# Optimization experiments

Hardware: AMD Instinct MI355X
Metric: run time of the kernel (lower is better)

Reference implementation:

```python
import jax, jax.numpy as jnp
import numpy as np

D_SINGLE = 384
D_PAIR = 128
D_HID = 16
H = 12
PQ = 4
PV = 8
EPS = 1e-8


def setup_inputs() -> dict:
    key = jax.random.key(0)
    ks = jax.random.split(key, 12)
    B, N = 1, 768
    w = lambda k, shp: jax.random.normal(k, shp, dtype=jnp.float32) * 0.02
    hc = H * D_HID
    concat_dim = H * (D_PAIR + D_HID + PV * 4)
    return {
        's': jax.random.normal(ks[0], (B, N, D_SINGLE), dtype=jnp.float32),
        'z': jax.random.normal(ks[1], (B, N, N, D_PAIR), dtype=jnp.float32),
        'square_mask': jnp.zeros((B, 1, N, N), dtype=jnp.float32),
        'rot': jax.random.normal(ks[2], (B, N, 3, 3), dtype=jnp.float32),
        'trans': jax.random.normal(ks[3], (B, N, 3), dtype=jnp.float32),
        'Wq': w(ks[4], (D_SINGLE, hc)), 'bq': jnp.zeros((hc,), jnp.float32),
        'Wkv': w(ks[5], (D_SINGLE, 2 * hc)), 'bkv': jnp.zeros((2 * hc,), jnp.float32),
        'Wqp': w(ks[6], (D_SINGLE, H * PQ * 3)), 'bqp': jnp.zeros((H * PQ * 3,), jnp.float32),
        'Wkvp': w(ks[7], (D_SINGLE, H * (PQ + PV) * 3)), 'bkvp': jnp.zeros((H * (PQ + PV) * 3,), jnp.float32),
        'Wb': w(ks[8], (D_PAIR, H)), 'bb': jnp.zeros((H,), jnp.float32),
        'head_weights': jnp.zeros((H,), jnp.float32),
        'Wout': w(ks[9], (concat_dim, D_SINGLE)), 'bout': jnp.zeros((D_SINGLE,), jnp.float32),
    }


def _ipa(s, z, square_mask, rot, trans, Wq, bq, Wkv, bkv, Wqp, bqp, Wkvp, bkvp,
         Wb, bb, head_weights, Wout, bout):
    B, N, _ = s.shape
    # scalar q/k/v
    q = (s @ Wq + bq).reshape(B, N, H, D_HID)
    kv = (s @ Wkv + bkv).reshape(B, N, H, 2 * D_HID)
    k, v = kv[..., :D_HID], kv[..., D_HID:]

    def frame_apply(pts):  # pts [B,N,K,3] -> R @ p + t per residue
        return jnp.einsum('bnij,bnkj->bnki', rot, pts) + trans[:, :, None, :]

    def to_points(raw):  # [B,N,3K] coordinate-major -> [B,N,K,3]
        x, y, zc = jnp.split(raw, 3, axis=-1)
        return jnp.stack([x, y, zc], axis=-1)

    q_pts = frame_apply(to_points(s @ Wqp + bqp)).reshape(B, N, H, PQ, 3)
    kv_pts = frame_apply(to_points(s @ Wkvp + bkvp)).reshape(B, N, H, PQ + PV, 3)
    k_pts, v_pts = kv_pts[..., :PQ, :], kv_pts[..., PQ:, :]

    # scalar attention + pair bias
    bias = z @ Wb + bb  # [B,N,N,H]
    attn = jnp.einsum('bqhd,bkhd->bhqk', q, k) * np.sqrt(1.0 / (3 * D_HID))
    attn = attn + np.sqrt(1.0 / 3) * jnp.transpose(bias, (0, 3, 1, 2))

    # point-distance attention
    diff = q_pts[:, :, None] - k_pts[:, None]          # [B,Nq,Nk,H,PQ,3]
    d2 = jnp.sum(diff * diff, axis=-1)                  # [B,Nq,Nk,H,PQ]
    hw = jax.nn.softplus(head_weights) * np.sqrt(1.0 / (3 * (PQ * 9.0 / 2)))
    pt_att = -0.5 * jnp.sum(d2 * hw[None, None, None, :, None], axis=-1)  # [B,Nq,Nk,H]

    attn = attn + square_mask + jnp.transpose(pt_att, (0, 3, 1, 2))
    attn = jax.nn.softmax(attn, axis=-1)                # [B,H,Nq,Nk]

    # aggregation
    o = jnp.einsum('bhqk,bkhd->bqhd', attn, v).reshape(B, N, H * D_HID)
    o_pts = jnp.einsum('bhqk,bkhpc->bqhpc', attn, v_pts)           # [B,N,H,PV,3]
    o_pair = jnp.einsum('bhqk,bqkc->bqhc', attn, z).reshape(B, N, H * D_PAIR)

    # invert frames: R^T (p - t)
    o_pts = jnp.einsum('bnji,bnhpj->bnhpi', rot, o_pts - trans[:, :, None, None, :])
    o_pts_norm = jnp.sqrt(jnp.sum(o_pts * o_pts, axis=-1) + EPS).reshape(B, N, H * PV)
    o_pts_flat = o_pts.reshape(B, N, H * PV, 3)

    cat = jnp.concatenate(
        [o, o_pts_flat[..., 0], o_pts_flat[..., 1], o_pts_flat[..., 2], o_pts_norm, o_pair],
        axis=-1)
    return cat @ Wout + bout


def reference(s, z, square_mask, rot, trans, Wq, bq, Wkv, bkv, Wqp, bqp, Wkvp,
              bkvp, Wb, bb, head_weights, Wout, bout):
    return _ipa(s, z, square_mask, rot, trans, Wq, bq, Wkv, bkv, Wqp, bqp,
                Wkvp, bkvp, Wb, bb, head_weights, Wout, bout)
```

## Files before the change

kernel.cpp:

```cpp
#include <hip/hip_runtime.h>
#include <hip/hip_bf16.h>
#include <math.h>

#define N_RES 768
#define DS 384
#define DP 128
#define DH 16
#define NH 12
#define PQ 4
#define PV 8
#define HC (NH*DH)
#define CATD (NH*(DP+DH+PV*4))
#define BK 64
#define NSPLIT 2
#define KRANGE (N_RES/NSPLIT)
#define PSTRIDE 2048
#define ZST 140

typedef __attribute__((ext_vector_type(8))) short bf16x8;
typedef __attribute__((ext_vector_type(4))) float f32x4;

#define WS_Q     0
#define WS_KT    (WS_Q + N_RES*HC)
#define WS_QP    (WS_KT + NH*N_RES*DH)
#define WS_KPT   (WS_QP + N_RES*144)
#define WS_KPSQ  (WS_KPT + NH*N_RES*12)
#define WS_RAWQ  (WS_KPSQ + NH*N_RES)
#define WS_RAWKV (WS_RAWQ + N_RES*144)
#define WS_VT    (WS_RAWKV + N_RES*432)
#define WS_VPT   (WS_VT + 192*N_RES/2)
#define WS_CATB  (WS_VPT + 288*N_RES/2)
#define WS_WOT   (WS_CATB + N_RES*CATD/2)
#define WS_PART  (WS_WOT + 384*CATD/2)
#define WS_SB    (WS_PART + N_RES*NSPLIT*PSTRIDE)
#define WS_WT    (WS_SB + 768*384/2)
#define WS_QA    (WS_WT + 1152*384/2)
#define WS_KB    (WS_QA + NH*N_RES*32/2)
#define WS_SP    (WS_KB + NH*N_RES*32/2)

__device__ __forceinline__ unsigned short f2b(float f) {
    union { __hip_bfloat16 b; unsigned short u; } c;
    c.b = __float2bfloat16(f);
    return c.u;
}
__device__ __forceinline__ float b2f(unsigned short u) {
    return __uint_as_float((unsigned)u << 16);
}

__global__ __launch_bounds__(384) void k_cvtall(
    const float* __restrict__ s,
    const float* __restrict__ Wq, const float* __restrict__ Wkv,
    const float* __restrict__ Wqp, const float* __restrict__ Wkvp,
    const float* __restrict__ Wout, float* __restrict__ ws)
{
    const int b = blockIdx.x, t = threadIdx.x;
    unsigned short* sb  = (unsigned short*)(ws + WS_SB);
    unsigned short* wt  = (unsigned short*)(ws + WS_WT);
    unsigned short* wot = (unsigned short*)(ws + WS_WOT);
    if (b < 768) {
        sb[(size_t)b * 384 + t] = f2b(s[(size_t)b * 384 + t]);
    } else if (b < 1920) {
        int j = b - 768;
        const float* W; int col, nc;
        if (j < 192)      { W = Wq;   col = j;       nc = 192; }
        else if (j < 576) { W = Wkv;  col = j - 192; nc = 384; }
        else if (j < 720) { W = Wqp;  col = j - 576; nc = 144; }
        else              { W = Wkvp; col = j - 720; nc = 432; }
        wt[(size_t)j * 384 + t] = f2b(W[(size_t)t * nc + col]);
    } else {
        int k = b - 1920;
        wot[(size_t)t * CATD + k] = f2b(Wout[(size_t)k * DS + t]);
    }
}

__global__ __launch_bounds__(256) void k_projm(
    const float* __restrict__ bq, const float* __restrict__ bkv,
    const float* __restrict__ bqp, const float* __restrict__ bkvp,
    float* __restrict__ ws)
{
    __shared__ float red[16][96];
    const int t = threadIdx.x;
    const int lane = t & 63;
    const int w = t >> 6;
    const int l15 = lane & 15;
    const int g = lane >> 4;
    const int m0 = blockIdx.x * 16;
    const int j0 = blockIdx.y * 96;
    const unsigned short* sb = (const unsigned short*)(ws + WS_SB);
    const unsigned short* wt = (const unsigned short*)(ws + WS_WT);
    unsigned short* vt = (unsigned short*)(ws + WS_VT);

    f32x4 acc[6];
    #pragma unroll
    for (int i = 0; i < 6; i++) acc[i] = (f32x4){0.f, 0.f, 0.f, 0.f};

    for (int ks = w; ks < 12; ks += 4) {
        int k0 = ks * 32;
        bf16x8 a = *(const bf16x8*)&sb[(size_t)(m0 + l15) * 384 + k0 + g * 8];
        #pragma unroll
        for (int ns = 0; ns < 6; ns++) {
            bf16x8 bfr = *(const bf16x8*)&wt[(size_t)(j0 + ns * 16 + l15) * 384 + k0 + g * 8];
            acc[ns] = __builtin_amdgcn_mfma_f32_16x16x32_bf16(a, bfr, acc[ns], 0, 0, 0);
        }
    }
    for (int idx = t; idx < 16 * 96; idx += 256) ((float*)red)[idx] = 0.f;
    __syncthreads();
    #pragma unroll
    for (int ns = 0; ns < 6; ns++)
        #pragma unroll
        for (int r = 0; r < 4; r++)
            atomicAdd(&red[g * 4 + r][ns * 16 + l15], acc[ns][r]);
    __syncthreads();

    for (int idx = t; idx < 16 * 96; idx += 256) {
        int row = idx / 96, c = idx % 96;
        int n = m0 + row, j = j0 + c;
        float v = red[row][c];
        if (j < 192) {
            ws[WS_Q + (size_t)n * HC + j] = v + bq[j];
        } else if (j < 576) {
            int jj = j - 192, h = jj / 32, dd = jj % 32;
            float vb = v + bkv[jj];
            if (dd < 16) ws[WS_KT + ((size_t)h * N_RES + n) * 16 + dd] = vb;
            else         vt[(size_t)(h * 16 + dd - 16) * N_RES + n] = f2b(vb);
        } else if (j < 720) {
            ws[WS_RAWQ + (size_t)n * 144 + (j - 576)] = v + bqp[j - 576];
        } else {
            ws[WS_RAWKV + (size_t)n * 432 + (j - 720)] = v + bkvp[j - 720];
        }
    }
}

__global__ __launch_bounds__(192) void k_frame(
    const float* __restrict__ rot, const float* __restrict__ trans,
    const float* __restrict__ hweights,
    float* __restrict__ ws)
{
    __shared__ float kpsq_s[NH];
    __shared__ float qp_f[144];
    __shared__ float kp_f[144];
    const int n = blockIdx.x;
    const int t = threadIdx.x;
    unsigned short* vpt = (unsigned short*)(ws + WS_VPT);
    unsigned short* qa  = (unsigned short*)(ws + WS_QA);
    unsigned short* kb  = (unsigned short*)(ws + WS_KB);
    if (t < NH) kpsq_s[t] = 0.f;
    __syncthreads();
    const float* R = rot + n * 9;
    const float* T = trans + n * 3;
    if (t < 48) {
        float x = ws[WS_RAWQ + (size_t)n * 144 + t];
        float y = ws[WS_RAWQ + (size_t)n * 144 + 48 + t];
        float z = ws[WS_RAWQ + (size_t)n * 144 + 96 + t];
        qp_f[t * 3 + 0] = R[0] * x + R[1] * y + R[2] * z + T[0];
        qp_f[t * 3 + 1] = R[3] * x + R[4] * y + R[5] * z + T[1];
        qp_f[t * 3 + 2] = R[6] * x + R[7] * y + R[8] * z + T[2];
    } else {
        int p2 = t - 48;
        float x = ws[WS_RAWKV + (size_t)n * 432 + p2];
        float y = ws[WS_RAWKV + (size_t)n * 432 + 144 + p2];
        float z = ws[WS_RAWKV + (size_t)n * 432 + 288 + p2];
        int h = p2 / 12, pp = p2 % 12;
        float fx = R[0] * x + R[1] * y + R[2] * z + T[0];
        float fy = R[3] * x + R[4] * y + R[5] * z + T[1];
        float fz = R[6] * x + R[7] * y + R[8] * z + T[2];
        if (pp < 4) {
            kp_f[h * 12 + pp * 3 + 0] = fx;
            kp_f[h * 12 + pp * 3 + 1] = fy;
            kp_f[h * 12 + pp * 3 + 2] = fz;
            atomicAdd(&kpsq_s[h], fx * fx + fy * fy + fz * fz);
        } else {
            size_t b = (size_t)(h * 24 + (pp - 4) * 3) * N_RES + n;
            vpt[b] = f2b(fx); vpt[b + N_RES] = f2b(fy); vpt[b + 2 * N_RES] = f2b(fz);
        }
    }
    __syncthreads();
    if (t < NH) ws[WS_KPSQ + (size_t)t * N_RES + n] = kpsq_s[t];
    for (int i = t; i < 768; i += 192) {
        int side = i / 384, idx = i % 384;
        int h = idx / 32, c = idx % 32;
        if (side == 0) {
            float hwv = log1pf(expf(hweights[h])) * 0.1360827635f;
            float v = (c < 16) ? ws[WS_Q + (size_t)n * HC + h * 16 + c] * 0.1443375673f
                    : ((c < 28) ? qp_f[h * 12 + (c - 16)] * hwv : 0.f);
            qa[((size_t)h * N_RES + n) * 32 + c] = f2b(v);
        } else {
            float v = (c < 16) ? ws[WS_KT + ((size_t)h * N_RES + n) * 16 + c]
                    : ((c < 28) ? kp_f[h * 12 + (c - 16)] : 0.f);
            kb[((size_t)h * N_RES + n) * 32 + c] = f2b(v);
        }
    }
}

__global__ __launch_bounds__(256) void k_logit(
    const float* __restrict__ mask, const float* __restrict__ bb,
    const float* __restrict__ hweights, float* __restrict__ ws)
{
    const int t = threadIdx.x;
    const int lane = t & 63;
    const int w = t >> 6;
    const int l15 = lane & 15;
    const int g = lane >> 4;
    const int q0 = blockIdx.x * 64 + w * 16;
    const int k0 = blockIdx.y * 96;
    const int h  = blockIdx.z;
    const unsigned short* qa = (const unsigned short*)(ws + WS_QA);
    const unsigned short* kb = (const unsigned short*)(ws + WS_KB);
    unsigned short* sp = (unsigned short*)(ws + WS_SP);

    float hwv = log1pf(expf(hweights[h])) * 0.1360827635f;
    float bbt = bb[h] * 0.5773502692f;

    bf16x8 a = *(const bf16x8*)&qa[((size_t)h * N_RES + q0 + l15) * 32 + g * 8];
    f32x4 acc[6];
    #pragma unroll
    for (int ns = 0; ns < 6; ns++) {
        bf16x8 bf = *(const bf16x8*)&kb[((size_t)h * N_RES + k0 + ns * 16 + l15) * 32 + g * 8];
        acc[ns] = __builtin_amdgcn_mfma_f32_16x16x32_bf16(
            a, bf, (f32x4){0.f, 0.f, 0.f, 0.f}, 0, 0, 0);
    }
    #pragma unroll
    for (int ns = 0; ns < 6; ns++) {
        int kk = k0 + ns * 16 + l15;
        float kq = ws[WS_KPSQ + (size_t)h * N_RES + kk];
        #pragma unroll
        for (int r = 0; r < 4; r++) {
            int qq = q0 + g * 4 + r;
            float v = acc[ns][r] + mask[(size_t)qq * N_RES + kk] + bbt - 0.5f * hwv * kq;
            sp[((size_t)h * N_RES + qq) * N_RES + kk] = f2b(v);
        }
    }
}

__global__ __launch_bounds__(256) void k_attn(
    const float* __restrict__ zg, const float* __restrict__ Wb,
    float* __restrict__ ws)
{
    __shared__ unsigned short z_s[2][BK][ZST];
    __shared__ unsigned short wb_lds[4][64][8];
    __shared__ unsigned short p_lds[16][72];
    __shared__ float b_lds[BK][13];
    __shared__ float r_s[16];

    const int t = threadIdx.x;
    const int lane = t & 63;
    const int w = t >> 6;
    const int l15 = lane & 15;
    const int g = lane >> 4;
    const int h0 = 3 * w;
    const int q  = blockIdx.x >> 1;
    const int ks = blockIdx.x & 1;
    const int kbase = ks * KRANGE;

    const float* zq = zg + ((size_t)q * N_RES + kbase) * DP;
    const unsigned short* VT  = (const unsigned short*)(ws + WS_VT);
    const unsigned short* VPT = (const unsigned short*)(ws + WS_VPT);
    const unsigned short* sp  = (const unsigned short*)(ws + WS_SP);

    for (int i = t; i < 16 * 72; i += 256) p_lds[i / 72][i % 72] = 0;
    if (t < 16) r_s[t] = 1.f;
    for (int i = t; i < 4 * 64 * 8; i += 256) {
        int j = i & 7, ln = (i >> 3) & 63, kc = i >> 9;
        int c = kc * 32 + ((ln >> 4) << 3) + j;
        int h = ln & 15;
        wb_lds[kc][ln][j] = (h < 12) ? f2b(Wb[c * NH + h] * 0.5773502692f)
                                     : (unsigned short)0;
    }
    {
        const float4* src = (const float4*)zq;
        #pragma unroll
        for (int i = 0; i < 8; i++) {
            int idx = i * 256 + t;
            float4 v = src[idx];
            unsigned u0 = (unsigned)f2b(v.x) | ((unsigned)f2b(v.y) << 16);
            unsigned u1 = (unsigned)f2b(v.z) | ((unsigned)f2b(v.w) << 16);
            *(unsigned long long*)&z_s[0][idx >> 5][(idx & 31) * 4] =
                (unsigned long long)u0 | ((unsigned long long)u1 << 32);
        }
    }

    float m_run[3], ssum[3];
    #pragma unroll
    for (int hl = 0; hl < 3; hl++) { m_run[hl] = -1e30f; ssum[hl] = 0.f; }

    f32x4 acc_op[2], acc_o[3], acc_pt[5];
    #pragma unroll
    for (int i = 0; i < 2; i++) acc_op[i] = (f32x4){0.f, 0.f, 0.f, 0.f};
    #pragma unroll
    for (int i = 0; i < 3; i++) acc_o[i] = (f32x4){0.f, 0.f, 0.f, 0.f};
    #pragma unroll
    for (int i = 0; i < 5; i++) acc_pt[i] = (f32x4){0.f, 0.f, 0.f, 0.f};

    __syncthreads();

    int cur = 0;
    for (int kb = 0; kb < KRANGE; kb += BK) {
        {
            f32x4 bacc = (f32x4){0.f, 0.f, 0.f, 0.f};
            #pragma unroll
            for (int kc = 0; kc < 4; kc++) {
                bf16x8 a = *(bf16x8*)&wb_lds[kc][lane][0];
                bf16x8 b = *(bf16x8*)&z_s[cur][w * 16 + l15][kc * 32 + g * 8];
                bacc = __builtin_amdgcn_mfma_f32_16x16x32_bf16(a, b, bacc, 0, 0, 0);
            }
            #pragma unroll
            for (int r = 0; r < 4; r++) {
                int h = g * 4 + r;
                if (h < 12) b_lds[w * 16 + l15][h] = bacc[r];
            }
        }
        __syncthreads();

        {
            const int kk = kbase + kb + lane;
            #pragma unroll
            for (int hl = 0; hl < 3; hl++) {
                int gh = h0 + hl;
                float dot = b_lds[lane][gh]
                          + b2f(sp[((size_t)gh * N_RES + q) * N_RES + kk]);
                float lm = dot;
                #pragma unroll
                for (int off = 32; off; off >>= 1) lm = fmaxf(lm, __shfl_xor(lm, off));
                float m_new = fmaxf(m_run[hl], lm);
                float rr = __expf(m_run[hl] - m_new);
                float p = __expf(dot - m_new);
                ssum[hl] = ssum[hl] * rr + p;
                m_run[hl] = m_new;
                p_lds[gh][lane] = f2b(p);
                if (lane == 0) r_s[gh] = rr;
            }
        }
        __syncthreads();

        const bool has_next = (kb + BK < KRANGE);
        const float4* src = (const float4*)(zq + (size_t)(kb + BK) * DP);
        float4 va[4];
        if (has_next) {
            #pragma unroll
            for (int i = 0; i < 4; i++) va[i] = src[i * 256 + t];
        }
        {
            bf16x8 pa0 = *(bf16x8*)&p_lds[l15][g * 8];
            bf16x8 pa1 = *(bf16x8*)&p_lds[l15][32 + g * 8];
            float rr0 = r_s[g * 4 + 0], rr1 = r_s[g * 4 + 1];
            float rr2 = r_s[g * 4 + 2], rr3 = r_s[g * 4 + 3];

            #pragma unroll
            for (int i = 0; i < 2; i++) {
                int c = (w * 2 + i) * 16 + l15;
                acc_op[i][0] *= rr0; acc_op[i][1] *= rr1;
                acc_op[i][2] *= rr2; acc_op[i][3] *= rr3;
                union { bf16x8 v; unsigned short u[8]; } b0, b1;
                #pragma unroll
                for (int j = 0; j < 8; j++) {
                    b0.u[j] = z_s[cur][g * 8 + j][c];
                    b1.u[j] = z_s[cur][32 + g * 8 + j][c];
                }
                acc_op[i] = __builtin_amdgcn_mfma_f32_16x16x32_bf16(pa0, b0.v, acc_op[i], 0, 0, 0);
                acc_op[i] = __builtin_amdgcn_mfma_f32_16x16x32_bf16(pa1, b1.v, acc_op[i], 0, 0, 0);
            }
            #pragma unroll
            for (int i = 0; i < 3; i++) {
                int vtile = w * 3 + i;
                acc_o[i][0] *= rr0; acc_o[i][1] *= rr1;
                acc_o[i][2] *= rr2; acc_o[i][3] *= rr3;
                const unsigned short* vr = VT + (size_t)(vtile * 16 + l15) * N_RES + kbase + kb;
                bf16x8 b0 = *(const bf16x8*)&vr[g * 8];
                bf16x8 b1 = *(const bf16x8*)&vr[32 + g * 8];
                acc_o[i] = __builtin_amdgcn_mfma_f32_16x16x32_bf16(pa0, b0, acc_o[i], 0, 0, 0);
                acc_o[i] = __builtin_amdgcn_mfma_f32_16x16x32_bf16(pa1, b1, acc_o[i], 0, 0, 0);
            }
            if (has_next) {
                #pragma unroll
                for (int i = 0; i < 4; i++) {
                    int idx = i * 256 + t;
                    float4 v = va[i];
                    unsigned u0 = (unsigned)f2b(v.x) | ((unsigned)f2b(v.y) << 16);
                    unsigned u1 = (unsigned)f2b(v.z) | ((unsigned)f2b(v.w) << 16);
                    *(unsigned long long*)&z_s[cur ^ 1][idx >> 5][(idx & 31) * 4] =
                        (unsigned long long)u0 | ((unsigned long long)u1 << 32);
                }
                #pragma unroll
                for (int i = 0; i < 4; i++) va[i] = src[(4 + i) * 256 + t];
            }
            #pragma unroll
            for (int i = 0; i < 5; i++) {
                int pt = w * 5 + i;
                if (pt < 18) {
                    acc_pt[i][0] *= rr0; acc_pt[i][1] *= rr1;
                    acc_pt[i][2] *= rr2; acc_pt[i][3] *= rr3;
                    const unsigned short* vr = VPT + (size_t)(pt * 16 + l15) * N_RES + kbase + kb;
                    bf16x8 b0 = *(const bf16x8*)&vr[g * 8];
                    bf16x8 b1 = *(const bf16x8*)&vr[32 + g * 8];
                    acc_pt[i] = __builtin_amdgcn_mfma_f32_16x16x32_bf16(pa0, b0, acc_pt[i], 0, 0, 0);
                    acc_pt[i] = __builtin_amdgcn_mfma_f32_16x16x32_bf16(pa1, b1, acc_pt[i], 0, 0, 0);
                }
            }
            if (has_next) {
                #pragma unroll
                for (int i = 0; i < 4; i++) {
                    int idx = (4 + i) * 256 + t;
                    float4 v = va[i];
                    unsigned u0 = (unsigned)f2b(v.x) | ((unsigned)f2b(v.y) << 16);
                    unsigned u1 = (unsigned)f2b(v.z) | ((unsigned)f2b(v.w) << 16);
                    *(unsigned long long*)&z_s[cur ^ 1][idx >> 5][(idx & 31) * 4] =
                        (unsigned long long)u0 | ((unsigned long long)u1 << 32);
                }
            }
        }
        __syncthreads();
        cur ^= 1;
    }

    float svv[3];
    #pragma unroll
    for (int hl = 0; hl < 3; hl++) {
        float sv = ssum[hl];
        #pragma unroll
        for (int off = 32; off; off >>= 1) sv += __shfl_xor(sv, off);
        svv[hl] = sv;
    }
    float* part = ws + WS_PART + (size_t)blockIdx.x * PSTRIDE;
    if (lane == 0) {
        #pragma unroll
        for (int hl = 0; hl < 3; hl++) {
            part[h0 + hl] = m_run[hl];
            part[12 + h0 + hl] = svv[hl];
        }
    }
    #pragma unroll
    for (int i = 0; i < 2; i++) {
        int c = (w * 2 + i) * 16 + l15;
        #pragma unroll
        for (int r = 0; r < 4; r++) {
            int h = g * 4 + r;
            if (h < 12) part[504 + h * 128 + c] = acc_op[i][r];
        }
    }
    #pragma unroll
    for (int i = 0; i < 3; i++) {
        int vtile = w * 3 + i;
        #pragma unroll
        for (int r = 0; r < 4; r++) {
            if ((vtile & 3) == r && (vtile >> 2) == g)
                part[24 + vtile * 16 + l15] = acc_o[i][r];
        }
    }
    #pragma unroll
    for (int i = 0; i < 5; i++) {
        int pt = w * 5 + i;
        if (pt < 18) {
            int pcol = pt * 16 + l15;
            int hown = pcol / 24;
            #pragma unroll
            for (int r = 0; r < 4; r++) {
                if (hown == g * 4 + r) part[216 + pcol] = acc_pt[i][r];
            }
        }
    }
}

__global__ __launch_bounds__(256) void k_merge(
    const float* __restrict__ rot, const float* __restrict__ trans,
    float* __restrict__ ws)
{
    __shared__ float w_s[NSPLIT][NH];
    __shared__ float opts_s[288];
    __shared__ float rot_s[9], trans_s[3];
    const int t = threadIdx.x;
    const int q = blockIdx.x;
    const float* P0 = ws + WS_PART + (size_t)q * NSPLIT * PSTRIDE;
    unsigned short* catb = (unsigned short*)(ws + WS_CATB) + (size_t)q * CATD;

    if (t < NH) {
        float m0 = P0[t], m1 = P0[PSTRIDE + t];
        float M = fmaxf(m0, m1);
        float e0 = __expf(m0 - M), e1 = __expf(m1 - M);
        float denom = e0 * P0[12 + t] + e1 * P0[PSTRIDE + 12 + t];
        float inv = 1.f / denom;
        w_s[0][t] = e0 * inv; w_s[1][t] = e1 * inv;
    }
    if (t < 9) rot_s[t] = rot[q * 9 + t];
    if (t < 3) trans_s[t] = trans[q * 3 + t];
    __syncthreads();

    for (int e = t; e < 2016; e += 256) {
        int h, po;
        if (e < 192)      { h = e >> 4;          po = 24 + e; }
        else if (e < 480) { h = (e - 192) / 24;  po = 216 + (e - 192); }
        else              { h = (e - 480) >> 7;  po = 504 + (e - 480); }
        float val = w_s[0][h] * P0[po] + w_s[1][h] * P0[PSTRIDE + po];
        if (e < 192)      catb[e] = f2b(val);
        else if (e < 480) opts_s[e - 192] = val;
        else              catb[576 + (e - 480)] = f2b(val);
    }
    __syncthreads();

    if (t < 96) {
        int gh = t >> 3, p = t & 7;
        float gx = opts_s[gh * 24 + p * 3 + 0] - trans_s[0];
        float gy = opts_s[gh * 24 + p * 3 + 1] - trans_s[1];
        float gz = opts_s[gh * 24 + p * 3 + 2] - trans_s[2];
        float lx = rot_s[0] * gx + rot_s[3] * gy + rot_s[6] * gz;
        float ly = rot_s[1] * gx + rot_s[4] * gy + rot_s[7] * gz;
        float lz = rot_s[2] * gx + rot_s[5] * gy + rot_s[8] * gz;
        catb[192 + t] = f2b(lx);
        catb[288 + t] = f2b(ly);
        catb[384 + t] = f2b(lz);
        catb[480 + t] = f2b(sqrtf(lx * lx + ly * ly + lz * lz + 1e-8f));
    }
}

__global__ __launch_bounds__(256) void k_out(
    const float* __restrict__ ws, const float* __restrict__ bout,
    float* __restrict__ out)
{
    __shared__ float red[16][96];
    const int t = threadIdx.x;
    const int lane = t & 63;
    const int w = t >> 6;
    const int l15 = lane & 15;
    const int g = lane >> 4;
    const int mt = blockIdx.x;
    const int n0 = blockIdx.y * 96;
    const unsigned short* catb = (const unsigned short*)(ws + WS_CATB);
    const unsigned short* wot  = (const unsigned short*)(ws + WS_WOT);

    f32x4 acc[6];
    #pragma unroll
    for (int i = 0; i < 6; i++) acc[i] = (f32x4){0.f, 0.f, 0.f, 0.f};

    for (int ks = w; ks < 66; ks += 4) {
        int k0 = ks * 32;
        bf16x8 a = *(const bf16x8*)&catb[(size_t)(mt * 16 + l15) * CATD + k0 + g * 8];
        #pragma unroll
        for (int ns = 0; ns < 6; ns++) {
            bf16x8 b = *(const bf16x8*)&wot[(size_t)(n0 + ns * 16 + l15) * CATD + k0 + g * 8];
            acc[ns] = __builtin_amdgcn_mfma_f32_16x16x32_bf16(a, b, acc[ns], 0, 0, 0);
        }
    }
    for (int idx = t; idx < 16 * 96; idx += 256) ((float*)red)[idx] = 0.f;
    __syncthreads();
    #pragma unroll
    for (int ns = 0; ns < 6; ns++)
        #pragma unroll
        for (int r = 0; r < 4; r++)
            atomicAdd(&red[g * 4 + r][ns * 16 + l15], acc[ns][r]);
    __syncthreads();
    for (int idx = t; idx < 16 * 96; idx += 256) {
        int row = idx / 96, c = idx % 96;
        out[(size_t)(mt * 16 + row) * DS + n0 + c] = red[row][c] + bout[n0 + c];
    }
}

extern "C" void kernel_launch(void* const* d_in, const int* in_sizes, int n_in,
                              void* d_out, int out_size, void* d_ws, size_t ws_size,
                              hipStream_t stream)
{
    const float* s     = (const float*)d_in[0];
    const float* z     = (const float*)d_in[1];
    const float* mask  = (const float*)d_in[2];
    const float* rot   = (const float*)d_in[3];
    const float* trans = (const float*)d_in[4];
    const float* Wq    = (const float*)d_in[5];
    const float* bq    = (const float*)d_in[6];
    const float* Wkv   = (const float*)d_in[7];
    const float* bkv   = (const float*)d_in[8];
    const float* Wqp   = (const float*)d_in[9];
    const float* bqp   = (const float*)d_in[10];
    const float* Wkvp  = (const float*)d_in[11];
    const float* bkvp  = (const float*)d_in[12];
    const float* Wb    = (const float*)d_in[13];
    const float* bb    = (const float*)d_in[14];
    const float* hwt   = (const float*)d_in[15];
    const float* Wout  = (const float*)d_in[16];
    const float* bout  = (const float*)d_in[17];
    float* ws  = (float*)d_ws;
    float* out = (float*)d_out;

    hipLaunchKernelGGL(k_cvtall, dim3(4032), dim3(384), 0, stream,
                       s, Wq, Wkv, Wqp, Wkvp, Wout, ws);
    hipLaunchKernelGGL(k_projm, dim3(48, 12), dim3(256), 0, stream,
                       bq, bkv, bqp, bkvp, ws);
    hipLaunchKernelGGL(k_frame, dim3(768), dim3(192), 0, stream, rot, trans, hwt, ws);
    hipLaunchKernelGGL(k_logit, dim3(12, 8, 12), dim3(256), 0, stream,
                       mask, bb, hwt, ws);
    hipLaunchKernelGGL(k_attn, dim3(N_RES * NSPLIT), dim3(256), 0, stream,
                       z, Wb, ws);
    hipLaunchKernelGGL(k_merge, dim3(N_RES), dim3(256), 0, stream, rot, trans, ws);
    hipLaunchKernelGGL(k_out, dim3(48, 4), dim3(256), 0, stream, ws, bout, out);
}
```

Before: 255.8 us.

## Drop split-K attention and fuse merge/frame-inversion epilogue into attention kernel

The attention kernel now processes all 768 keys per query in a single block instead of two half-range blocks, so it normalizes the softmax itself and writes bf16 outputs straight into the concat buffer. The point-frame inversion and norm from the separate merge kernel move into its epilogue, which removes one launch and the fp32 partial-result round trip through memory. The prefetch of the next z tile is also issued earlier, before the bias MFMA. In exchange the grid halves to 768 blocks, which lowers parallelism and occupancy on a large GPU and makes each block's serial loop twice as long.

```diff
diff --git a/kernel.cpp b/kernel.cpp
--- a/kernel.cpp
+++ b/kernel.cpp
@@ -12,9 +12,6 @@
 #define HC (NH*DH)
 #define CATD (NH*(DP+DH+PV*4))
 #define BK 64
-#define NSPLIT 2
-#define KRANGE (N_RES/NSPLIT)
-#define PSTRIDE 2048
 #define ZST 140
 
 typedef __attribute__((ext_vector_type(8))) short bf16x8;
@@ -32,7 +29,7 @@
 #define WS_CATB  (WS_VPT + 288*N_RES/2)
 #define WS_WOT   (WS_CATB + N_RES*CATD/2)
 #define WS_PART  (WS_WOT + 384*CATD/2)
-#define WS_SB    (WS_PART + N_RES*NSPLIT*PSTRIDE)
+#define WS_SB    (WS_PART + N_RES*2*2048)
 #define WS_WT    (WS_SB + 768*384/2)
 #define WS_QA    (WS_WT + 1152*384/2)
 #define WS_KB    (WS_QA + NH*N_RES*32/2)
@@ -234,13 +231,16 @@
 
 __global__ __launch_bounds__(256) void k_attn(
     const float* __restrict__ zg, const float* __restrict__ Wb,
+    const float* __restrict__ rot, const float* __restrict__ trans,
     float* __restrict__ ws)
 {
     __shared__ unsigned short z_s[2][BK][ZST];
     __shared__ unsigned short wb_lds[4][64][8];
     __shared__ unsigned short p_lds[16][72];
     __shared__ float b_lds[BK][13];
-    __shared__ float r_s[16];
+    __shared__ float r_s[16], inv_s[16];
+    __shared__ float opts_s[288];
+    __shared__ float rot_s[9], trans_s[3];
 
     const int t = threadIdx.x;
     const int lane = t & 63;
@@ -248,17 +248,18 @@
     const int l15 = lane & 15;
     const int g = lane >> 4;
     const int h0 = 3 * w;
-    const int q  = blockIdx.x >> 1;
-    const int ks = blockIdx.x & 1;
-    const int kbase = ks * KRANGE;
-
-    const float* zq = zg + ((size_t)q * N_RES + kbase) * DP;
+    const int q = blockIdx.x;
+
+    const float* zq = zg + (size_t)q * N_RES * DP;
     const unsigned short* VT  = (const unsigned short*)(ws + WS_VT);
     const unsigned short* VPT = (const unsigned short*)(ws + WS_VPT);
     const unsigned short* sp  = (const unsigned short*)(ws + WS_SP);
+    unsigned short* catb = (unsigned short*)(ws + WS_CATB) + (size_t)q * CATD;
 
     for (int i = t; i < 16 * 72; i += 256) p_lds[i / 72][i % 72] = 0;
-    if (t < 16) r_s[t] = 1.f;
+    if (t < 16) { r_s[t] = 1.f; inv_s[t] = 1.f; }
+    if (t < 9) rot_s[t] = rot[q * 9 + t];
+    if (t < 3) trans_s[t] = trans[q * 3 + t];
     for (int i = t; i < 4 * 64 * 8; i += 256) {
         int j = i & 7, ln = (i >> 3) & 63, kc = i >> 9;
         int c = kc * 32 + ((ln >> 4) << 3) + j;
@@ -294,7 +295,15 @@
     __syncthreads();
 
     int cur = 0;
-    for (int kb = 0; kb < KRANGE; kb += BK) {
+    for (int kb = 0; kb < N_RES; kb += BK) {
+        const bool has_next = (kb + BK < N_RES);
+        const float4* src = (const float4*)(zq + (size_t)(kb + BK) * DP);
+        float4 va[4];
+        if (has_next) {
+            #pragma unroll
+            for (int i = 0; i < 4; i++) va[i] = src[i * 256 + t];
+        }
+
         {
             f32x4 bacc = (f32x4){0.f, 0.f, 0.f, 0.f};
             #pragma unroll
@@ -312,7 +321,7 @@
         __syncthreads();
 
         {
-            const int kk = kbase + kb + lane;
+            const int kk = kb + lane;
             #pragma unroll
             for (int hl = 0; hl < 3; hl++) {
                 int gh = h0 + hl;
@@ -332,13 +341,6 @@
         }
         __syncthreads();
 
-        const bool has_next = (kb + BK < KRANGE);
-        const float4* src = (const float4*)(zq + (size_t)(kb + BK) * DP);
-        float4 va[4];
-        if (has_next) {
-            #pragma unroll
-            for (int i = 0; i < 4; i++) va[i] = src[i * 256 + t];
-        }
         {
             bf16x8 pa0 = *(bf16x8*)&p_lds[l15][g * 8];
             bf16x8 pa1 = *(bf16x8*)&p_lds[l15][32 + g * 8];
@@ -364,7 +366,7 @@
                 int vtile = w * 3 + i;
                 acc_o[i][0] *= rr0; acc_o[i][1] *= rr1;
                 acc_o[i][2] *= rr2; acc_o[i][3] *= rr3;
-                const unsigned short* vr = VT + (size_t)(vtile * 16 + l15) * N_RES + kbase + kb;
+                const unsigned short* vr = VT + (size_t)(vtile * 16 + l15) * N_RES + kb;
                 bf16x8 b0 = *(const bf16x8*)&vr[g * 8];
                 bf16x8 b1 = *(const bf16x8*)&vr[32 + g * 8];
                 acc_o[i] = __builtin_amdgcn_mfma_f32_16x16x32_bf16(pa0, b0, acc_o[i], 0, 0, 0);
@@ -389,7 +391,7 @@
                 if (pt < 18) {
                     acc_pt[i][0] *= rr0; acc_pt[i][1] *= rr1;
                     acc_pt[i][2] *= rr2; acc_pt[i][3] *= rr3;
-                    const unsigned short* vr = VPT + (size_t)(pt * 16 + l15) * N_RES + kbase + kb;
+                    const unsigned short* vr = VPT + (size_t)(pt * 16 + l15) * N_RES + kb;
                     bf16x8 b0 = *(const bf16x8*)&vr[g * 8];
                     bf16x8 b1 = *(const bf16x8*)&vr[32 + g * 8];
                     acc_pt[i] = __builtin_amdgcn_mfma_f32_16x16x32_bf16(pa0, b0, acc_pt[i], 0, 0, 0);
@@ -412,29 +414,24 @@
         cur ^= 1;
     }
 
-    float svv[3];
+    float inv3[3];
     #pragma unroll
     for (int hl = 0; hl < 3; hl++) {
         float sv = ssum[hl];
         #pragma unroll
         for (int off = 32; off; off >>= 1) sv += __shfl_xor(sv, off);
-        svv[hl] = sv;
-    }
-    float* part = ws + WS_PART + (size_t)blockIdx.x * PSTRIDE;
-    if (lane == 0) {
-        #pragma unroll
-        for (int hl = 0; hl < 3; hl++) {
-            part[h0 + hl] = m_run[hl];
-            part[12 + h0 + hl] = svv[hl];
-        }
-    }
+        inv3[hl] = 1.f / sv;
+        if (lane == 0) inv_s[h0 + hl] = inv3[hl];
+    }
+    __syncthreads();
+
     #pragma unroll
     for (int i = 0; i < 2; i++) {
         int c = (w * 2 + i) * 16 + l15;
         #pragma unroll
         for (int r = 0; r < 4; r++) {
             int h = g * 4 + r;
-            if (h < 12) part[504 + h * 128 + c] = acc_op[i][r];
+            if (h < 12) catb[576 + h * 128 + c] = f2b(acc_op[i][r] * inv_s[h]);
         }
     }
     #pragma unroll
@@ -443,7 +440,7 @@
         #pragma unroll
         for (int r = 0; r < 4; r++) {
             if ((vtile & 3) == r && (vtile >> 2) == g)
-                part[24 + vtile * 16 + l15] = acc_o[i][r];
+                catb[vtile * 16 + l15] = f2b(acc_o[i][r] * inv_s[vtile]);
         }
     }
     #pragma unroll
@@ -454,45 +451,9 @@
             int hown = pcol / 24;
             #pragma unroll
             for (int r = 0; r < 4; r++) {
-                if (hown == g * 4 + r) part[216 + pcol] = acc_pt[i][r];
-            }
-        }
-    }
-}
-
-__global__ __launch_bounds__(256) void k_merge(
-    const float* __restrict__ rot, const float* __restrict__ trans,
-    float* __restrict__ ws)
-{
-    __shared__ float w_s[NSPLIT][NH];
-    __shared__ float opts_s[288];
-    __shared__ float rot_s[9], trans_s[3];
-    const int t = threadIdx.x;
-    const int q = blockIdx.x;
-    const float* P0 = ws + WS_PART + (size_t)q * NSPLIT * PSTRIDE;
-    unsigned short* catb = (unsigned short*)(ws + WS_CATB) + (size_t)q * CATD;
-
-    if (t < NH) {
-        float m0 = P0[t], m1 = P0[PSTRIDE + t];
-        float M = fmaxf(m0, m1);
-        float e0 = __expf(m0 - M), e1 = __expf(m1 - M);
-        float denom = e0 * P0[12 + t] + e1 * P0[PSTRIDE + 12 + t];
-        float inv = 1.f / denom;
-        w_s[0][t] = e0 * inv; w_s[1][t] = e1 * inv;
-    }
-    if (t < 9) rot_s[t] = rot[q * 9 + t];
-    if (t < 3) trans_s[t] = trans[q * 3 + t];
-    __syncthreads();
-
-    for (int e = t; e < 2016; e += 256) {
-        int h, po;
-        if (e < 192)      { h = e >> 4;          po = 24 + e; }
-        else if (e < 480) { h = (e - 192) / 24;  po = 216 + (e - 192); }
-        else              { h = (e - 480) >> 7;  po = 504 + (e - 480); }
-        float val = w_s[0][h] * P0[po] + w_s[1][h] * P0[PSTRIDE + po];
-        if (e < 192)      catb[e] = f2b(val);
-        else if (e < 480) opts_s[e - 192] = val;
-        else              catb[576 + (e - 480)] = f2b(val);
+                if (hown == g * 4 + r) opts_s[pcol] = acc_pt[i][r] * inv_s[hown];
+            }
+        }
     }
     __syncthreads();
 
@@ -585,8 +546,7 @@
     hipLaunchKernelGGL(k_frame, dim3(768), dim3(192), 0, stream, rot, trans, hwt, ws);
     hipLaunchKernelGGL(k_logit, dim3(12, 8, 12), dim3(256), 0, stream,
                        mask, bb, hwt, ws);
-    hipLaunchKernelGGL(k_attn, dim3(N_RES * NSPLIT), dim3(256), 0, stream,
-                       z, Wb, ws);
-    hipLaunchKernelGGL(k_merge, dim3(N_RES), dim3(256), 0, stream, rot, trans, ws);
+    hipLaunchKernelGGL(k_attn, dim3(N_RES), dim3(256), 0, stream,
+                       z, Wb, rot, trans, ws);
     hipLaunchKernelGGL(k_out, dim3(48, 4), dim3(256), 0, stream, ws, bout, out);
 }
```

After: 275.1 us. 7.5% more time.

## Split value and point aggregation out of attention kernel into separate pass

Applied to the files above, without the earlier changes.

The attention kernel no longer aggregates scalar values and value points. Instead it writes the bf16 logits to a new workspace buffer, and the merge kernel stores the per-row max and inverse denominator. A new kernel recomputes the normalized probabilities from the stored logits and runs per-head MFMA products against V and the value points, then applies the inverse frame transform. This cuts register and MFMA pressure in the z-streaming attention loop, at the cost of an extra kernel launch and about 14 MB of logit writes plus reads.

```diff
diff --git a/kernel.cpp b/kernel.cpp
--- a/kernel.cpp
+++ b/kernel.cpp
@@ -37,6 +37,9 @@
 #define WS_QA    (WS_WT + 1152*384/2)
 #define WS_KB    (WS_QA + NH*N_RES*32/2)
 #define WS_SP    (WS_KB + NH*N_RES*32/2)
+#define WS_SL    (WS_SP + NH*N_RES*N_RES/2)
+#define WS_MF    (WS_SL + NH*N_RES*N_RES/2)
+#define WS_IV    (WS_MF + NH*N_RES)
 
 __device__ __forceinline__ unsigned short f2b(float f) {
     union { __hip_bfloat16 b; unsigned short u; } c;
@@ -253,9 +256,8 @@
     const int kbase = ks * KRANGE;
 
     const float* zq = zg + ((size_t)q * N_RES + kbase) * DP;
-    const unsigned short* VT  = (const unsigned short*)(ws + WS_VT);
-    const unsigned short* VPT = (const unsigned short*)(ws + WS_VPT);
-    const unsigned short* sp  = (const unsigned short*)(ws + WS_SP);
+    const unsigned short* sp = (const unsigned short*)(ws + WS_SP);
+    unsigned short* sl = (unsigned short*)(ws + WS_SL);
 
     for (int i = t; i < 16 * 72; i += 256) p_lds[i / 72][i % 72] = 0;
     if (t < 16) r_s[t] = 1.f;
@@ -283,17 +285,14 @@
     #pragma unroll
     for (int hl = 0; hl < 3; hl++) { m_run[hl] = -1e30f; ssum[hl] = 0.f; }
 
-    f32x4 acc_op[2], acc_o[3], acc_pt[5];
+    f32x4 acc_op[2];
     #pragma unroll
     for (int i = 0; i < 2; i++) acc_op[i] = (f32x4){0.f, 0.f, 0.f, 0.f};
-    #pragma unroll
-    for (int i = 0; i < 3; i++) acc_o[i] = (f32x4){0.f, 0.f, 0.f, 0.f};
-    #pragma unroll
-    for (int i = 0; i < 5; i++) acc_pt[i] = (f32x4){0.f, 0.f, 0.f, 0.f};
 
     __syncthreads();
 
     int cur = 0;
+    #pragma unroll 1
     for (int kb = 0; kb < KRANGE; kb += BK) {
         {
             f32x4 bacc = (f32x4){0.f, 0.f, 0.f, 0.f};
@@ -318,6 +317,7 @@
                 int gh = h0 + hl;
                 float dot = b_lds[lane][gh]
                           + b2f(sp[((size_t)gh * N_RES + q) * N_RES + kk]);
+                sl[((size_t)gh * N_RES + q) * N_RES + kk] = f2b(dot);
                 float lm = dot;
                 #pragma unroll
                 for (int off = 32; off; off >>= 1) lm = fmaxf(lm, __shfl_xor(lm, off));
@@ -359,17 +359,6 @@
                 acc_op[i] = __builtin_amdgcn_mfma_f32_16x16x32_bf16(pa0, b0.v, acc_op[i], 0, 0, 0);
                 acc_op[i] = __builtin_amdgcn_mfma_f32_16x16x32_bf16(pa1, b1.v, acc_op[i], 0, 0, 0);
             }
-            #pragma unroll
-            for (int i = 0; i < 3; i++) {
-                int vtile = w * 3 + i;
-                acc_o[i][0] *= rr0; acc_o[i][1] *= rr1;
-                acc_o[i][2] *= rr2; acc_o[i][3] *= rr3;
-                const unsigned short* vr = VT + (size_t)(vtile * 16 + l15) * N_RES + kbase + kb;
-                bf16x8 b0 = *(const bf16x8*)&vr[g * 8];
-                bf16x8 b1 = *(const bf16x8*)&vr[32 + g * 8];
-                acc_o[i] = __builtin_amdgcn_mfma_f32_16x16x32_bf16(pa0, b0, acc_o[i], 0, 0, 0);
-                acc_o[i] = __builtin_amdgcn_mfma_f32_16x16x32_bf16(pa1, b1, acc_o[i], 0, 0, 0);
-            }
             if (has_next) {
                 #pragma unroll
                 for (int i = 0; i < 4; i++) {
@@ -382,21 +371,6 @@
                 }
                 #pragma unroll
                 for (int i = 0; i < 4; i++) va[i] = src[(4 + i) * 256 + t];
-            }
-            #pragma unroll
-            for (int i = 0; i < 5; i++) {
-                int pt = w * 5 + i;
-                if (pt < 18) {
-                    acc_pt[i][0] *= rr0; acc_pt[i][1] *= rr1;
-                    acc_pt[i][2] *= rr2; acc_pt[i][3] *= rr3;
-                    const unsigned short* vr = VPT + (size_t)(pt * 16 + l15) * N_RES + kbase + kb;
-                    bf16x8 b0 = *(const bf16x8*)&vr[g * 8];
-                    bf16x8 b1 = *(const bf16x8*)&vr[32 + g * 8];
-                    acc_pt[i] = __builtin_amdgcn_mfma_f32_16x16x32_bf16(pa0, b0, acc_pt[i], 0, 0, 0);
-                    acc_pt[i] = __builtin_amdgcn_mfma_f32_16x16x32_bf16(pa1, b1, acc_pt[i], 0, 0, 0);
-                }
-            }
-            if (has_next) {
                 #pragma unroll
                 for (int i = 0; i < 4; i++) {
                     int idx = (4 + i) * 256 + t;
@@ -437,36 +411,11 @@
             if (h < 12) part[504 + h * 128 + c] = acc_op[i][r];
         }
     }
-    #pragma unroll
-    for (int i = 0; i < 3; i++) {
-        int vtile = w * 3 + i;
-        #pragma unroll
-        for (int r = 0; r < 4; r++) {
-            if ((vtile & 3) == r && (vtile >> 2) == g)
-                part[24 + vtile * 16 + l15] = acc_o[i][r];
-        }
-    }
-    #pragma unroll
-    for (int i = 0; i < 5; i++) {
-        int pt = w * 5 + i;
-        if (pt < 18) {
-            int pcol = pt * 16 + l15;
-            int hown = pcol / 24;
-            #pragma unroll
-            for (int r = 0; r < 4; r++) {
-                if (hown == g * 4 + r) part[216 + pcol] = acc_pt[i][r];
-            }
-        }
-    }
-}
-
-__global__ __launch_bounds__(256) void k_merge(
-    const float* __restrict__ rot, const float* __restrict__ trans,
-    float* __restrict__ ws)
+}
+
+__global__ __launch_bounds__(256) void k_merge(float* __restrict__ ws)
 {
     __shared__ float w_s[NSPLIT][NH];
-    __shared__ float opts_s[288];
-    __shared__ float rot_s[9], trans_s[3];
     const int t = threadIdx.x;
     const int q = blockIdx.x;
     const float* P0 = ws + WS_PART + (size_t)q * NSPLIT * PSTRIDE;
@@ -479,35 +428,87 @@
         float denom = e0 * P0[12 + t] + e1 * P0[PSTRIDE + 12 + t];
         float inv = 1.f / denom;
         w_s[0][t] = e0 * inv; w_s[1][t] = e1 * inv;
-    }
-    if (t < 9) rot_s[t] = rot[q * 9 + t];
-    if (t < 3) trans_s[t] = trans[q * 3 + t];
-    __syncthreads();
-
-    for (int e = t; e < 2016; e += 256) {
-        int h, po;
-        if (e < 192)      { h = e >> 4;          po = 24 + e; }
-        else if (e < 480) { h = (e - 192) / 24;  po = 216 + (e - 192); }
-        else              { h = (e - 480) >> 7;  po = 504 + (e - 480); }
+        ws[WS_MF + (size_t)t * N_RES + q] = M;
+        ws[WS_IV + (size_t)t * N_RES + q] = inv;
+    }
+    __syncthreads();
+
+    for (int e = t; e < 1536; e += 256) {
+        int h = e >> 7, po = 504 + e;
         float val = w_s[0][h] * P0[po] + w_s[1][h] * P0[PSTRIDE + po];
-        if (e < 192)      catb[e] = f2b(val);
-        else if (e < 480) opts_s[e - 192] = val;
-        else              catb[576 + (e - 480)] = f2b(val);
-    }
-    __syncthreads();
-
-    if (t < 96) {
-        int gh = t >> 3, p = t & 7;
-        float gx = opts_s[gh * 24 + p * 3 + 0] - trans_s[0];
-        float gy = opts_s[gh * 24 + p * 3 + 1] - trans_s[1];
-        float gz = opts_s[gh * 24 + p * 3 + 2] - trans_s[2];
-        float lx = rot_s[0] * gx + rot_s[3] * gy + rot_s[6] * gz;
-        float ly = rot_s[1] * gx + rot_s[4] * gy + rot_s[7] * gz;
-        float lz = rot_s[2] * gx + rot_s[5] * gy + rot_s[8] * gz;
-        catb[192 + t] = f2b(lx);
-        catb[288 + t] = f2b(ly);
-        catb[384 + t] = f2b(lz);
-        catb[480 + t] = f2b(sqrtf(lx * lx + ly * ly + lz * lz + 1e-8f));
+        catb[576 + e] = f2b(val);
+    }
+}
+
+__global__ __launch_bounds__(256) void k_ov(
+    const float* __restrict__ rot, const float* __restrict__ trans,
+    float* __restrict__ ws)
+{
+    __shared__ float red[16][48];
+    const int t = threadIdx.x;
+    const int lane = t & 63;
+    const int w = t >> 6;
+    const int l15 = lane & 15;
+    const int g = lane >> 4;
+    const int q0 = blockIdx.x * 16;
+    const int h  = blockIdx.y;
+    const unsigned short* sl  = (const unsigned short*)(ws + WS_SL);
+    const unsigned short* VT  = (const unsigned short*)(ws + WS_VT);
+    const unsigned short* VPT = (const unsigned short*)(ws + WS_VPT);
+    unsigned short* catb = (unsigned short*)(ws + WS_CATB);
+
+    const float Mq = ws[WS_MF + (size_t)h * N_RES + q0 + l15];
+    const float iq = ws[WS_IV + (size_t)h * N_RES + q0 + l15];
+
+    f32x4 acc[3];
+    #pragma unroll
+    for (int i = 0; i < 3; i++) acc[i] = (f32x4){0.f, 0.f, 0.f, 0.f};
+
+    for (int kc = w; kc < 24; kc += 4) {
+        int k0 = kc * 32 + g * 8;
+        const unsigned short* lr = sl + ((size_t)h * N_RES + q0 + l15) * N_RES + k0;
+        union { bf16x8 v; unsigned short u[8]; } pa;
+        #pragma unroll
+        for (int j = 0; j < 8; j++)
+            pa.u[j] = f2b(__expf(b2f(lr[j]) - Mq) * iq);
+        bf16x8 b0 = *(const bf16x8*)&VT[(size_t)(h * 16 + l15) * N_RES + k0];
+        bf16x8 b1 = *(const bf16x8*)&VPT[(size_t)(h * 24 + l15) * N_RES + k0];
+        bf16x8 b2 = *(const bf16x8*)&VPT[(size_t)(h * 24 + 16 + l15) * N_RES + k0];
+        acc[0] = __builtin_amdgcn_mfma_f32_16x16x32_bf16(pa.v, b0, acc[0], 0, 0, 0);
+        acc[1] = __builtin_amdgcn_mfma_f32_16x16x32_bf16(pa.v, b1, acc[1], 0, 0, 0);
+        acc[2] = __builtin_amdgcn_mfma_f32_16x16x32_bf16(pa.v, b2, acc[2], 0, 0, 0);
+    }
+    for (int i = t; i < 16 * 48; i += 256) ((float*)red)[i] = 0.f;
+    __syncthreads();
+    #pragma unroll
+    for (int r = 0; r < 4; r++) {
+        int row = g * 4 + r;
+        atomicAdd(&red[row][l15], acc[0][r]);
+        atomicAdd(&red[row][16 + l15], acc[1][r]);
+        if (l15 < 8) atomicAdd(&red[row][32 + l15], acc[2][r]);
+    }
+    __syncthreads();
+
+    {
+        int qq = q0 + (t >> 4), d = t & 15;
+        catb[(size_t)qq * CATD + h * 16 + d] = f2b(red[t >> 4][d]);
+    }
+    if (t < 128) {
+        int ql = t >> 3, p = t & 7;
+        int qq = q0 + ql;
+        const float* R = rot + qq * 9;
+        const float* T = trans + qq * 3;
+        float gx = red[ql][16 + p * 3 + 0] - T[0];
+        float gy = red[ql][16 + p * 3 + 1] - T[1];
+        float gz = red[ql][16 + p * 3 + 2] - T[2];
+        float lx = R[0] * gx + R[3] * gy + R[6] * gz;
+        float ly = R[1] * gx + R[4] * gy + R[7] * gz;
+        float lz = R[2] * gx + R[5] * gy + R[8] * gz;
+        unsigned short* cb = catb + (size_t)qq * CATD;
+        cb[192 + h * 8 + p] = f2b(lx);
+        cb[288 + h * 8 + p] = f2b(ly);
+        cb[384 + h * 8 + p] = f2b(lz);
+        cb[480 + h * 8 + p] = f2b(sqrtf(lx * lx + ly * ly + lz * lz + 1e-8f));
     }
 }
 
@@ -587,6 +588,7 @@
                        mask, bb, hwt, ws);
     hipLaunchKernelGGL(k_attn, dim3(N_RES * NSPLIT), dim3(256), 0, stream,
                        z, Wb, ws);
-    hipLaunchKernelGGL(k_merge, dim3(N_RES), dim3(256), 0, stream, rot, trans, ws);
+    hipLaunchKernelGGL(k_merge, dim3(N_RES), dim3(256), 0, stream, ws);
+    hipLaunchKernelGGL(k_ov, dim3(48, 12), dim3(256), 0, stream, rot, trans, ws);
     hipLaunchKernelGGL(k_out, dim3(48, 4), dim3(256), 0, stream, ws, bout, out);
 }
```

After: 213.3 us. 1.2x faster.
